# Kernel tuning notes

Measured on AMD Instinct MI355X. Metric: run time of the kernel, lower is better.

Reference implementation:

```python
import jax, jax.numpy as jnp
from jax import lax
import numpy as np

GRID, IMG, BLOCK = 60, 960, 16
BN_EPS = 1e-5


def _conv(x, w, b):
    return lax.conv_general_dilated(x, w, (1, 1), 'SAME', dimension_numbers=('NCHW', 'OIHW', 'NCHW')) + b[None, :, None, None]


def _bn(x, g, b):
    # inference BatchNorm with running_mean=0, running_var=1
    s = g * np.float32(1.0 / np.sqrt(1.0 + BN_EPS))
    return x * s[None, :, None, None] + b[None, :, None, None]


def _mlp(x, w1, b1, w2, b2):
    return jax.nn.relu(x @ w1.T + b1) @ w2.T + b2


def _lstm_layer(x, wih, whh, b):
    # x: [B,T,D]; torch gate order i,f,g,o; zero initial state
    B = x.shape[0]
    H = whh.shape[1]
    pre = jnp.swapaxes(x, 0, 1) @ wih.T + b  # [T,B,4H]

    def step(carry, p):
        h, c = carry
        z = p + h @ whh.T
        i, f, g, o = jnp.split(z, 4, axis=-1)
        c = jax.nn.sigmoid(f) * c + jax.nn.sigmoid(i) * jnp.tanh(g)
        h = jax.nn.sigmoid(o) * jnp.tanh(c)
        return (h, c), h

    z0 = jnp.zeros((B, H), x.dtype)
    (h, c), ys = lax.scan(step, (z0, z0), pre)
    return jnp.swapaxes(ys, 0, 1), h, c


def _forward(motion_vectors, boxes, track_ids, conv1_w, conv1_b, bn1_g, bn1_b, conv2_w, conv2_b, bn2_g, bn2_b, conv3_w, conv3_b, bn3_g, bn3_b, agg_w1, agg_b1, agg_w2, agg_b2, bx_w1, bx_b1, bx_w2, bx_b2, id_table, proj_w, proj_b, empty_slot, l0_wih, l0_whh, l0_b, l1_wih, l1_whh, l1_b, hb_w1, hb_b1, hb_w2, hb_b2, hc_w1, hc_b1, hc_w2, hc_b2, ht_w1, ht_b1, ht_w2, ht_b2):
    B = motion_vectors.shape[0]
    # ---- grid encoder (Conv-BN-ReLU x3) ----
    x = jax.nn.relu(_bn(_conv(motion_vectors, conv1_w, conv1_b), bn1_g, bn1_b))
    x = jax.nn.relu(_bn(_conv(x, conv2_w, conv2_b), bn2_g, bn2_b))
    gf = jax.nn.relu(_bn(_conv(x, conv3_w, conv3_b), bn3_g, bn3_b))  # [B,64,60,60]
    global_feat = gf.mean((-2, -1))  # AdaptiveAvgPool2d(1) -> [B,64]

    # ---- per-box motion statistics (vectorized masked reductions) ----
    bg = jnp.clip(boxes * (IMG / BLOCK), 0.0, GRID - 1e-6)  # grid coords
    ix1 = jnp.floor(bg[..., 0]); iy1 = jnp.floor(bg[..., 1])
    ix2 = jnp.maximum(ix1 + 1.0, jnp.ceil(bg[..., 2]))
    iy2 = jnp.maximum(iy1 + 1.0, jnp.ceil(bg[..., 3]))
    g = jnp.arange(GRID, dtype=bg.dtype)
    mx_ = (g >= ix1[..., None]) & (g < ix2[..., None])  # [B,N,60]
    my_ = (g >= iy1[..., None]) & (g < iy2[..., None])
    mask = my_[..., :, None] & mx_[..., None, :]  # [B,N,60,60]
    m = mask.astype(bg.dtype)
    cnt = m.sum((-2, -1))[..., None]  # [B,N,1], >= 1 by construction
    mv = motion_vectors  # [B,2,60,60]
    s1 = jnp.einsum('bnyx,bcyx->bnc', m, mv)
    s2 = jnp.einsum('bnyx,bcyx->bnc', m, mv * mv)
    mean = s1 / cnt
    var = (s2 - cnt * mean * mean) / jnp.maximum(cnt - 1.0, 1.0)  # unbiased, like torch .std()
    var_safe = jnp.where(cnt > 1.0, jnp.maximum(var, 1e-12), 1.0)
    std = jnp.where(cnt > 1.0, jnp.sqrt(var_safe), 0.0)
    BIG = jnp.asarray(1e9, bg.dtype)
    mn = jnp.min(jnp.where(mask[:, :, None], mv[:, None], BIG), axis=(-2, -1))   # [B,N,2]
    mx = jnp.max(jnp.where(mask[:, :, None], mv[:, None], -BIG), axis=(-2, -1))  # [B,N,2]
    stats = jnp.stack([mean[..., 0], mean[..., 1], std[..., 0], std[..., 1], mn[..., 0], mx[..., 0], mn[..., 1], mx[..., 1]], -1)  # [B,N,8]
    motion_emb = _mlp(stats, agg_w1, agg_b1, agg_w2, agg_b2)  # [B,N,64]

    # ---- slot initialization ----
    box_emb = _mlp(boxes, bx_w1, bx_b1, bx_w2, bx_b2)  # [B,N,64]
    id_emb = id_table[jnp.clip(track_ids, 0, 999)]  # [B,N,32]
    obj = jnp.concatenate([box_emb, id_emb, motion_emb], -1)  # [B,N,160]
    slots = obj @ proj_w.T + proj_b  # [B,300,128]; N == max_slots so no empty slots used

    # ---- 2-layer LSTM over the 300 slots (batch_first, eval -> no dropout) ----
    Ns = slots.shape[1]
    gexp = jnp.broadcast_to(global_feat[:, None, :], (B, Ns, global_feat.shape[-1]))
    lstm_in = jnp.concatenate([slots, gexp], -1)  # [B,300,192]
    y, h0, c0 = _lstm_layer(lstm_in, l0_wih, l0_whh, l0_b)
    y, h1, c1 = _lstm_layer(y, l1_wih, l1_whh, l1_b)  # [B,300,128]

    # ---- RT-DETR style heads ----
    pred_boxes = jax.nn.sigmoid(_mlp(y, hb_w1, hb_b1, hb_w2, hb_b2))  # [B,300,4]
    cls_logits = _mlp(y, hc_w1, hc_b1, hc_w2, hc_b2)  # [B,300,2]
    tid_logits = _mlp(y, ht_w1, ht_b1, ht_w2, ht_b2)  # [B,300,1000]
    h = jnp.stack([h0, h1])
    c = jnp.stack([c0, c1])
    return pred_boxes, cls_logits, tid_logits, h, c


def setup_inputs() -> dict:
    B, N = 32, 300
    key = jax.random.key(0)
    ks = iter(jax.random.split(key, 60))

    def w(*s):
        return jax.random.normal(next(ks), s, jnp.float32) * 0.05

    mv = jax.random.normal(next(ks), (B, 2, GRID, GRID), jnp.float32)
    bb = jax.random.uniform(next(ks), (B, N, 4), jnp.float32)
    boxes = jnp.concatenate([jnp.minimum(bb[..., :2], bb[..., 2:]), jnp.maximum(bb[..., :2], bb[..., 2:])], -1)
    track_ids = jax.random.randint(next(ks), (B, N), 0, 1000)
    return dict(
        motion_vectors=mv, boxes=boxes, track_ids=track_ids,
        conv1_w=w(32, 2, 3, 3), conv1_b=w(32), bn1_g=1.0 + w(32), bn1_b=w(32),
        conv2_w=w(64, 32, 3, 3), conv2_b=w(64), bn2_g=1.0 + w(64), bn2_b=w(64),
        conv3_w=w(64, 64, 3, 3), conv3_b=w(64), bn3_g=1.0 + w(64), bn3_b=w(64),
        agg_w1=w(32, 8), agg_b1=w(32), agg_w2=w(64, 32), agg_b2=w(64),
        bx_w1=w(32, 4), bx_b1=w(32), bx_w2=w(64, 32), bx_b2=w(64),
        id_table=w(1000, 32).at[0].set(0.0),
        proj_w=w(128, 160), proj_b=w(128), empty_slot=w(128),
        l0_wih=w(512, 192), l0_whh=w(512, 128), l0_b=w(512),
        l1_wih=w(512, 128), l1_whh=w(512, 128), l1_b=w(512),
        hb_w1=w(256, 128), hb_b1=w(256), hb_w2=w(4, 256), hb_b2=w(4),
        hc_w1=w(256, 128), hc_b1=w(256), hc_w2=w(2, 256), hc_b2=w(2),
        ht_w1=w(256, 128), ht_b1=w(256), ht_w2=w(1000, 256), ht_b2=w(1000))


def reference(motion_vectors, boxes, track_ids, conv1_w, conv1_b, bn1_g, bn1_b, conv2_w, conv2_b, bn2_g, bn2_b, conv3_w, conv3_b, bn3_g, bn3_b, agg_w1, agg_b1, agg_w2, agg_b2, bx_w1, bx_b1, bx_w2, bx_b2, id_table, proj_w, proj_b, empty_slot, l0_wih, l0_whh, l0_b, l1_wih, l1_whh, l1_b, hb_w1, hb_b1, hb_w2, hb_b2, hc_w1, hc_b1, hc_w2, hc_b2, ht_w1, ht_b1, ht_w2, ht_b2):
    return _forward(motion_vectors, boxes, track_ids, conv1_w, conv1_b, bn1_g, bn1_b, conv2_w, conv2_b, bn2_g, bn2_b, conv3_w, conv3_b, bn3_g, bn3_b, agg_w1, agg_b1, agg_w2, agg_b2, bx_w1, bx_b1, bx_w2, bx_b2, id_table, proj_w, proj_b, empty_slot, l0_wih, l0_whh, l0_b, l1_wih, l1_whh, l1_b, hb_w1, hb_b1, hb_w2, hb_b2, hc_w1, hc_b1, hc_w2, hc_b2, ht_w1, ht_b1, ht_w2, ht_b2)
```

## Files before the change

kernel.cpp:

```cpp
#include <hip/hip_runtime.h>
#include <hip/hip_bf16.h>
#include <math.h>

typedef unsigned short ushort_t;
typedef __attribute__((ext_vector_type(8))) short bf16x8;
typedef __attribute__((ext_vector_type(4))) float f32x4;

__device__ __forceinline__ float sigf(float x) {
  x = fminf(fmaxf(x, -30.f), 30.f);
  return 1.f / (1.f + __expf(-x));
}
__device__ __forceinline__ float sig2(float x) {
  return __builtin_amdgcn_rcpf(1.f + __expf(-x));
}
__device__ __forceinline__ float tanh2(float x) {
  return 1.f - 2.f * __builtin_amdgcn_rcpf(__expf(2.f * x) + 1.f);
}
__device__ __forceinline__ ushort_t f2bf(float x) {
  unsigned int b = __float_as_uint(x);
  unsigned int lsb = (b >> 16) & 1u;
  b += 0x7fffu + lsb;
  return (ushort_t)(b >> 16);
}
__device__ __forceinline__ float bf2f(ushort_t u) {
  return __uint_as_float(((unsigned int)u) << 16);
}

#define NPIX 3600
__device__ __forceinline__ int gperm(int rho) {
  return ((rho & 3) << 7) + (rho >> 2);
}

__global__ __launch_bounds__(256) void wprep_kernel(
    const float* __restrict__ conv2_w, const float* __restrict__ conv3_w,
    const float* __restrict__ wih0,
    const float* __restrict__ projW,
    const float* __restrict__ projb,
    const float* __restrict__ l0_b,
    const float* __restrict__ hbw1, const float* __restrict__ hcw1,
    const float* __restrict__ htw1, const float* __restrict__ htw2,
    const float* __restrict__ hbb1, const float* __restrict__ hcb1,
    const float* __restrict__ htb1, ushort_t* __restrict__ wc2,
    ushort_t* __restrict__ wc3, ushort_t* __restrict__ wAp,
    float* __restrict__ l0bp, ushort_t* __restrict__ whid,
    ushort_t* __restrict__ wt2, float* __restrict__ bhid) {
  int i = blockIdx.x * 256 + threadIdx.x;
  if (i < 18432) {
    int oc = i / 288, r = i % 288, kt = r / 32, ic = r % 32;
    wc2[i] = f2bf(conv2_w[((oc * 32 + ic) * 3 + kt / 3) * 3 + kt % 3]);
    return;
  }
  i -= 18432;
  if (i < 36864) {
    int oc = i / 576, r = i % 576, c = r / 288, r2 = r % 288;
    int kt = r2 / 32, icl = r2 % 32, ic = c * 32 + icl;
    wc3[i] = f2bf(conv3_w[((oc * 64 + ic) * 3 + kt / 3) * 3 + kt % 3]);
    return;
  }
  i -= 36864;
  if (i < 98304) {
    int n = i / 192, k = i % 192;
    int src = gperm(n);
    float a = 0.f;
    if (k < 160) {
      const float* wr = wih0 + src * 192;
      for (int j = 0; j < 128; ++j) a = fmaf(wr[j], projW[j * 160 + k], a);
    }
    wAp[i] = f2bf(a);
    return;
  }
  i -= 98304;
  if (i < 512) {
    int src = gperm(i);
    float a = l0_b[src];
    const float* wr = wih0 + src * 192;
    for (int j = 0; j < 128; ++j) a = fmaf(wr[j], projb[j], a);
    l0bp[i] = a;
    return;
  }
  i -= 512;
  if (i < 98304) {
    int row = i >> 7, c = i & 127;
    float v = (row < 256)   ? hbw1[row * 128 + c]
              : (row < 512) ? hcw1[(row - 256) * 128 + c]
                            : htw1[(row - 512) * 128 + c];
    whid[i] = f2bf(v);
    return;
  }
  i -= 98304;
  if (i < 256000) {
    wt2[i] = f2bf(htw2[i]);
    return;
  }
  i -= 256000;
  if (i < 768)
    bhid[i] = (i < 256) ? hbb1[i] : (i < 512) ? hcb1[i - 256] : htb1[i - 512];
}

__global__ __launch_bounds__(256) void gvec_kernel(
    const float* __restrict__ wih0, const float* __restrict__ gf,
    float* __restrict__ gvec) {
  int i = blockIdx.x * 256 + threadIdx.x;
  int b = i >> 9, n = i & 511;
  const float* wr = wih0 + gperm(n) * 192 + 128;
  const float* g = gf + b * 64;
  float a = 0.f;
#pragma unroll
  for (int k = 0; k < 64; ++k) a = fmaf(wr[k], g[k], a);
  gvec[i] = a * (1.f / 3600.f);
}

__global__ __launch_bounds__(256) void front_kernel(
    const float* __restrict__ mv, const float* __restrict__ c1w,
    const float* __restrict__ c1b, const float* __restrict__ bg1,
    const float* __restrict__ bb1, ushort_t* __restrict__ x1out,
    const float* __restrict__ boxes, const int* __restrict__ ids,
    const float* __restrict__ agg_w1, const float* __restrict__ agg_b1,
    const float* __restrict__ agg_w2, const float* __restrict__ agg_b2,
    const float* __restrict__ bx_w1, const float* __restrict__ bx_b1,
    const float* __restrict__ bx_w2, const float* __restrict__ bx_b2,
    const float* __restrict__ id_table, ushort_t* __restrict__ obj_out) {
  if (blockIdx.x < 14400) {
    int idx = blockIdx.x * 256 + threadIdx.x;
    int x = idx % 60;
    int y = (idx / 60) % 60;
    int oc = (idx / 3600) % 32;
    int b = idx / (3600 * 32);
    float acc = 0.f;
#pragma unroll
    for (int ic = 0; ic < 2; ++ic) {
      const float* src = mv + (b * 2 + ic) * NPIX;
      const float* wp = c1w + (oc * 2 + ic) * 9;
#pragma unroll
      for (int ky = 0; ky < 3; ++ky) {
        int gy = y + ky - 1;
        if (gy < 0 || gy >= 60) continue;
#pragma unroll
        for (int kx = 0; kx < 3; ++kx) {
          int gx = x + kx - 1;
          if (gx < 0 || gx >= 60) continue;
          acc = fmaf(src[gy * 60 + gx], wp[ky * 3 + kx], acc);
        }
      }
    }
    float s = bg1[oc] * rsqrtf(1.f + 1e-5f);
    float v = fmaf(acc, s, fmaf(c1b[oc], s, bb1[oc]));
    x1out[idx] = f2bf(fmaxf(v, 0.f));
    return;
  }
  __shared__ float obj[2][160];
  __shared__ float hm[2][32];
  __shared__ float hbx[2][32];
  __shared__ float stats[2][8];
  __shared__ float boxf[2][4];
  __shared__ float red[2][2][8];
  int h = threadIdx.x >> 7;
  int t = threadIdx.x & 127;
  int blk = (blockIdx.x - 14400) * 2 + h;
  int b = blk / 300;
  float bx0 = boxes[blk * 4 + 0], by0 = boxes[blk * 4 + 1];
  float bx1 = boxes[blk * 4 + 2], by1 = boxes[blk * 4 + 3];
  const float HI = (float)(60.0 - 1e-6);
  float gx1 = fminf(fmaxf(bx0 * 60.f, 0.f), HI);
  float gy1 = fminf(fmaxf(by0 * 60.f, 0.f), HI);
  float gx2 = fminf(fmaxf(bx1 * 60.f, 0.f), HI);
  float gy2 = fminf(fmaxf(by1 * 60.f, 0.f), HI);
  float fx1 = floorf(gx1), fy1 = floorf(gy1);
  float fx2 = fmaxf(fx1 + 1.f, ceilf(gx2));
  float fy2 = fmaxf(fy1 + 1.f, ceilf(gy2));
  int ix1 = (int)fx1, iy1 = (int)fy1, ix2 = (int)fx2, iy2 = (int)fy2;
  int w = ix2 - ix1, hgt = iy2 - iy1;
  int area = w * hgt;
  float s0 = 0.f, s1 = 0.f, q0 = 0.f, q1 = 0.f;
  float mn0 = 1e9f, mn1 = 1e9f, mx0 = -1e9f, mx1 = -1e9f;
  const float* mv0 = mv + b * 2 * NPIX;
  const float* mv1 = mv0 + NPIX;
  for (int i = t; i < area; i += 128) {
    int r = i / w, cc = i - r * w;
    int yy = iy1 + r, xx = ix1 + cc;
    float v0 = mv0[yy * 60 + xx];
    float v1 = mv1[yy * 60 + xx];
    s0 += v0; q0 += v0 * v0; mn0 = fminf(mn0, v0); mx0 = fmaxf(mx0, v0);
    s1 += v1; q1 += v1 * v1; mn1 = fminf(mn1, v1); mx1 = fmaxf(mx1, v1);
  }
#pragma unroll
  for (int off = 32; off; off >>= 1) {
    s0 += __shfl_down(s0, off); s1 += __shfl_down(s1, off);
    q0 += __shfl_down(q0, off); q1 += __shfl_down(q1, off);
    mn0 = fminf(mn0, __shfl_down(mn0, off));
    mn1 = fminf(mn1, __shfl_down(mn1, off));
    mx0 = fmaxf(mx0, __shfl_down(mx0, off));
    mx1 = fmaxf(mx1, __shfl_down(mx1, off));
  }
  if ((t & 63) == 0) {
    int wv = t >> 6;
    red[h][wv][0] = s0; red[h][wv][1] = s1;
    red[h][wv][2] = q0; red[h][wv][3] = q1;
    red[h][wv][4] = mn0; red[h][wv][5] = mn1;
    red[h][wv][6] = mx0; red[h][wv][7] = mx1;
  }
  __syncthreads();
  if (t == 0) {
    float S0 = red[h][0][0] + red[h][1][0], S1 = red[h][0][1] + red[h][1][1];
    float Q0 = red[h][0][2] + red[h][1][2], Q1 = red[h][0][3] + red[h][1][3];
    float MN0 = fminf(red[h][0][4], red[h][1][4]);
    float MN1 = fminf(red[h][0][5], red[h][1][5]);
    float MX0 = fmaxf(red[h][0][6], red[h][1][6]);
    float MX1 = fmaxf(red[h][0][7], red[h][1][7]);
    float cnt = (float)area;
    float mean0 = S0 / cnt, mean1 = S1 / cnt;
    float var0 = (Q0 - cnt * mean0 * mean0) / fmaxf(cnt - 1.f, 1.f);
    float var1 = (Q1 - cnt * mean1 * mean1) / fmaxf(cnt - 1.f, 1.f);
    float sd0 = (cnt > 1.f) ? sqrtf(fmaxf(var0, 1e-12f)) : 0.f;
    float sd1 = (cnt > 1.f) ? sqrtf(fmaxf(var1, 1e-12f)) : 0.f;
    stats[h][0] = mean0; stats[h][1] = mean1; stats[h][2] = sd0;
    stats[h][3] = sd1; stats[h][4] = MN0; stats[h][5] = MX0;
    stats[h][6] = MN1; stats[h][7] = MX1;
    boxf[h][0] = bx0; boxf[h][1] = by0; boxf[h][2] = bx1; boxf[h][3] = by1;
  }
  __syncthreads();
  if (t < 32) {
    float a = agg_b1[t];
#pragma unroll
    for (int k = 0; k < 8; ++k) a = fmaf(stats[h][k], agg_w1[t * 8 + k], a);
    hm[h][t] = fmaxf(a, 0.f);
  } else if (t < 64) {
    int j = t - 32;
    float a = bx_b1[j];
#pragma unroll
    for (int k = 0; k < 4; ++k) a = fmaf(boxf[h][k], bx_w1[j * 4 + k], a);
    hbx[h][j] = fmaxf(a, 0.f);
  }
  __syncthreads();
  if (t < 64) {
    float a = bx_b2[t];
#pragma unroll
    for (int k = 0; k < 32; ++k) a = fmaf(hbx[h][k], bx_w2[t * 32 + k], a);
    obj[h][t] = a;
  } else {
    int j = t - 64;
    float a = agg_b2[j];
#pragma unroll
    for (int k = 0; k < 32; ++k) a = fmaf(hm[h][k], agg_w2[j * 32 + k], a);
    obj[h][96 + j] = a;
  }
  if (t < 32) {
    int id = ids[blk];
    id = min(max(id, 0), 999);
    obj[h][64 + t] = id_table[id * 32 + t];
  }
  __syncthreads();
  obj_out[(size_t)blk * 192 + t] = f2bf(obj[h][t]);
  if (t < 32) {
    obj_out[(size_t)blk * 192 + 128 + t] = f2bf(obj[h][128 + t]);
    obj_out[(size_t)blk * 192 + 160 + t] = 0;
  }
}

template <int CIN, bool POOL>
__global__ __launch_bounds__(256) void conv_mfma_kernel(
    const ushort_t* __restrict__ in, const ushort_t* __restrict__ wc,
    const float* __restrict__ cb, const float* __restrict__ bg,
    const float* __restrict__ bb, ushort_t* __restrict__ out,
    float* __restrict__ gf) {
  constexpr int NCHUNK = CIN / 32;
  __shared__ ushort_t in_lds[18 * 18 * 40];
  int tid = threadIdx.x;
  int wv = tid >> 6, lane = tid & 63;
  int col = lane & 15, kg = lane >> 4;
  int b = blockIdx.y, tile = blockIdx.x;
  int tq = tile >> 2, tr = tile & 3;
  int ty0 = tq * 16 - (tq == 3 ? 4 : 0);
  int tx0 = tr * 16 - (tr == 3 ? 4 : 0);
  int oc = wv * 16 + col;

  bf16x8 bw[NCHUNK * 9];
#pragma unroll
  for (int c = 0; c < NCHUNK; ++c)
#pragma unroll
    for (int kt = 0; kt < 9; ++kt)
      bw[c * 9 + kt] = *(const bf16x8*)(wc + oc * (NCHUNK * 288) + c * 288 +
                                        kt * 32 + kg * 8);

  f32x4 acc[16];
#pragma unroll
  for (int m = 0; m < 16; ++m) acc[m] = (f32x4){0.f, 0.f, 0.f, 0.f};

  for (int c = 0; c < NCHUNK; ++c) {
    if (c) __syncthreads();
    for (int i = tid; i < 18 * 18 * 32; i += 256) {
      int ic = i / 324, rem = i % 324;
      int yy = rem / 18, xx = rem % 18;
      int gy = ty0 + yy - 1, gx = tx0 + xx - 1;
      ushort_t v = 0;
      if (gy >= 0 && gy < 60 && gx >= 0 && gx < 60)
        v = in[((size_t)(b * CIN + c * 32 + ic) * 60 + gy) * 60 + gx];
      in_lds[(yy * 18 + xx) * 40 + ic] = v;
    }
    __syncthreads();
#pragma unroll
    for (int kt = 0; kt < 9; ++kt) {
      int ky = kt / 3, kx = kt % 3;
#pragma unroll
      for (int m = 0; m < 16; ++m) {
        bf16x8 af =
            *(const bf16x8*)(&in_lds[((m + ky) * 18 + col + kx) * 40 + kg * 8]);
        acc[m] = __builtin_amdgcn_mfma_f32_16x16x32_bf16(af, bw[c * 9 + kt],
                                                         acc[m], 0, 0, 0);
      }
    }
  }
  float s = bg[oc] * rsqrtf(1.f + 1e-5f);
  float bias = fmaf(cb[oc], s, bb[oc]);
  float pool = 0.f;
#pragma unroll
  for (int m = 0; m < 16; ++m) {
    float vv[4];
#pragma unroll
    for (int r = 0; r < 4; ++r) vv[r] = fmaxf(fmaf(acc[m][r], s, bias), 0.f);
    if (POOL) {
      bool ymask = (tq != 3) || (m >= 4);
#pragma unroll
      for (int r = 0; r < 4; ++r) {
        int px = kg * 4 + r;
        bool xmask = (tr != 3) || (px >= 4);
        if (ymask && xmask) pool += vv[r];
      }
    } else {
      ushort_t st[4];
#pragma unroll
      for (int r = 0; r < 4; ++r) st[r] = f2bf(vv[r]);
      int yy = ty0 + m, xx = tx0 + kg * 4;
      *(uint2*)(&out[((size_t)(b * 64 + oc) * 60 + yy) * 60 + xx]) =
          *(uint2*)st;
    }
  }
  if (POOL) {
    pool += __shfl_xor(pool, 16);
    pool += __shfl_xor(pool, 32);
    if (lane < 16) atomicAdd(&gf[b * 64 + oc], pool);
  }
}

template <int ACT, bool OBF16, bool GVEC>
__global__ __launch_bounds__(256) void gemm_bf16w_kernel(
    const ushort_t* __restrict__ A, int lda, const ushort_t* __restrict__ W,
    const float* __restrict__ bias, void* __restrict__ C, int ldc, int M,
    int N, int K, const float* __restrict__ gvec) {
  __shared__ ushort_t As[128 * 64];
  __shared__ ushort_t Ws[64 * 64];
  int tid = threadIdx.x;
  int wv = tid >> 6, lane = tid & 63;
  int col = lane & 15, kg = lane >> 4;
  int wm = wv >> 1, wn = wv & 1;
  int m0 = blockIdx.x * 128, n0 = blockIdx.y * 64;
  f32x4 acc[4][2];
#pragma unroll
  for (int i = 0; i < 4; ++i)
#pragma unroll
    for (int j = 0; j < 2; ++j) acc[i][j] = (f32x4){0.f, 0.f, 0.f, 0.f};

  int nk = K >> 6;
  for (int kc = 0; kc < nk; ++kc) {
    if (kc) __syncthreads();
#pragma unroll
    for (int q = 0; q < 4; ++q) {
      int idx = q * 256 + tid;
      int row = idx >> 3, ch = idx & 7;
      uint4 v =
          *(const uint4*)(A + (size_t)(m0 + row) * lda + kc * 64 + ch * 8);
      *(uint4*)(&As[row * 64 + ((ch * 8) ^ ((row & 7) << 3))]) = v;
    }
#pragma unroll
    for (int q = 0; q < 2; ++q) {
      int idx = q * 256 + tid;
      int row = idx >> 3, ch = idx & 7;
      int n = n0 + row;
      uint4 v = make_uint4(0, 0, 0, 0);
      if (n < N) v = *(const uint4*)(W + (size_t)n * K + kc * 64 + ch * 8);
      *(uint4*)(&Ws[row * 64 + ((ch * 8) ^ ((row & 7) << 3))]) = v;
    }
    __syncthreads();
#pragma unroll
    for (int ks = 0; ks < 2; ++ks) {
      bf16x8 bfr[2], afr[4];
#pragma unroll
      for (int ni = 0; ni < 2; ++ni) {
        int row = wn * 32 + ni * 16 + col;
        bfr[ni] = *(const bf16x8*)(
            &Ws[row * 64 + ((ks * 32 + kg * 8) ^ ((row & 7) << 3))]);
      }
#pragma unroll
      for (int mi = 0; mi < 4; ++mi) {
        int row = wm * 64 + mi * 16 + col;
        afr[mi] = *(const bf16x8*)(
            &As[row * 64 + ((ks * 32 + kg * 8) ^ ((row & 7) << 3))]);
      }
#pragma unroll
      for (int mi = 0; mi < 4; ++mi)
#pragma unroll
        for (int ni = 0; ni < 2; ++ni)
          acc[mi][ni] = __builtin_amdgcn_mfma_f32_16x16x32_bf16(
              afr[mi], bfr[ni], acc[mi][ni], 0, 0, 0);
    }
  }
#pragma unroll
  for (int ni = 0; ni < 2; ++ni) {
    int n = n0 + wn * 32 + ni * 16 + col;
    float bn = (n < N) ? bias[n] : 0.f;
#pragma unroll
    for (int mi = 0; mi < 4; ++mi) {
      int mbase = m0 + wm * 64 + mi * 16 + kg * 4;
#pragma unroll
      for (int r = 0; r < 4; ++r) {
        float v = acc[mi][ni][r] + bn;
        if (GVEC) v += gvec[((mbase + r) / 300) * 512 + n];
        if (ACT == 1) v = fmaxf(v, 0.f);
        if (n < N) {
          if (OBF16)
            ((ushort_t*)C)[(size_t)(mbase + r) * ldc + n] = f2bf(v);
          else
            ((float*)C)[(size_t)(mbase + r) * ldc + n] = v;
        }
      }
    }
  }
}

__global__ __launch_bounds__(256) void head_small_kernel(
    const ushort_t* __restrict__ hid, const float* __restrict__ wb2,
    const float* __restrict__ bb2, const float* __restrict__ wc2,
    const float* __restrict__ bc2, float* __restrict__ outB,
    float* __restrict__ outC) {
  int idx = blockIdx.x * 256 + threadIdx.x;
  int row = idx / 6, j = idx % 6;
  const ushort_t* h = hid + (size_t)row * 768 + (j < 4 ? 0 : 256);
  const float* wrow = (j < 4) ? wb2 + j * 256 : wc2 + (j - 4) * 256;
  float acc = (j < 4) ? bb2[j] : bc2[j - 4];
  for (int k = 0; k < 256; k += 8) {
    uint4 hv = *(const uint4*)(h + k);
    unsigned int ww[4] = {hv.x, hv.y, hv.z, hv.w};
#pragma unroll
    for (int q = 0; q < 4; ++q) {
      acc = fmaf(bf2f((ushort_t)(ww[q] & 0xffff)), wrow[k + 2 * q], acc);
      acc = fmaf(bf2f((ushort_t)(ww[q] >> 16)), wrow[k + 2 * q + 1], acc);
    }
  }
  float v = (j < 4) ? sigf(acc) : acc;
  if (j < 4) outB[row * 4 + j] = v;
  else outC[row * 2 + (j - 4)] = v;
}

#define LSTM_BAR() asm volatile("s_waitcnt lgkmcnt(0)\n\ts_barrier" ::: "memory")

__global__ __launch_bounds__(512) void lstm_fused_kernel(
    const float* __restrict__ pre0,
    const float* __restrict__ whh0,
    const float* __restrict__ wih1,
    const float* __restrict__ whh1,
    const float* __restrict__ b1,
    float* __restrict__ pre1,
    ushort_t* __restrict__ y0,
    ushort_t* __restrict__ y1,
    float* __restrict__ outH, float* __restrict__ outC,
    unsigned int* __restrict__ flags)
{
  __shared__ ushort_t h_lds[2][4][160];
  int tid = threadIdx.x;
  int w = tid >> 6, lane = tid & 63;
  int col = lane & 15, kg = lane >> 4;
  int bat = col & 3, q = col >> 2;
  int cell = (4 * w + q) * 4 + kg;

  if (blockIdx.x < 8) {
    int g = blockIdx.x;
    int b0 = g * 4;
    unsigned int* flagp = &flags[g * 32];
    for (int i = tid; i < 2 * 4 * 160; i += 512) ((ushort_t*)h_lds)[i] = 0;
    bf16x8 aW0[4][4];
#pragma unroll
    for (int j = 0; j < 4; ++j) {
      int rho = (4 * w + j) * 16 + col;
      int src = gperm(rho);
#pragma unroll
      for (int kt = 0; kt < 4; ++kt) {
        const float* s1 = whh0 + src * 128 + kt * 32 + kg * 8;
        bf16x8 f1;
#pragma unroll
        for (int qq = 0; qq < 8; ++qq) f1[qq] = (short)f2bf(s1[qq]);
        aW0[j][kt] = f1;
      }
    }
    const float* pg = pre0 + (size_t)(b0 + bat) * 300 * 512 + 4 * cell;
    ushort_t* yg0 = y0 + ((size_t)(b0 + bat) * 300) * 128 + cell;
    float c = 0.f, hout = 0.f;
    f32x4 p0v = *(const f32x4*)(pg);
    f32x4 p1v = *(const f32x4*)(pg + 512);
    __syncthreads();

    for (int s = 0; s < 300; ++s) {
      const ushort_t* hb = h_lds[s & 1][bat];
      bf16x8 bfr[4];
#pragma unroll
      for (int kt = 0; kt < 4; ++kt)
        bfr[kt] = *(const bf16x8*)(hb + kt * 32 + kg * 8);
      f32x4 a0 = {0.f, 0.f, 0.f, 0.f}, a1 = a0, a2 = a0, a3 = a0;
#pragma unroll
      for (int kt = 0; kt < 4; ++kt) {
        a0 = __builtin_amdgcn_mfma_f32_16x16x32_bf16(aW0[0][kt], bfr[kt], a0, 0, 0, 0);
        a1 = __builtin_amdgcn_mfma_f32_16x16x32_bf16(aW0[1][kt], bfr[kt], a1, 0, 0, 0);
        a2 = __builtin_amdgcn_mfma_f32_16x16x32_bf16(aW0[2][kt], bfr[kt], a2, 0, 0, 0);
        a3 = __builtin_amdgcn_mfma_f32_16x16x32_bf16(aW0[3][kt], bfr[kt], a3, 0, 0, 0);
      }
      f32x4 z = a0;
      if (q == 1) z = a1;
      if (q == 2) z = a2;
      if (q == 3) z = a3;
      {
        float zi = z[0] + p0v[0];
        float zf = z[1] + p0v[1];
        float zg = z[2] + p0v[2];
        float zo = z[3] + p0v[3];
        float vi = sig2(zi), vf = sig2(zf), vg = tanh2(zg), vo = sig2(zo);
        c = vf * c + vi * vg;
        hout = vo * tanh2(c);
        ushort_t hv = f2bf(hout);
        h_lds[(s + 1) & 1][bat][cell] = hv;
        __builtin_nontemporal_store(hv, yg0 + (size_t)s * 128);
        p0v = p1v;
        int sn = (s + 2 < 300) ? s + 2 : 299;
        p1v = *(const f32x4*)(pg + (size_t)sn * 512);
      }
      asm volatile("s_waitcnt vmcnt(6)" ::: "memory");
      LSTM_BAR();
      if (tid == 0 && s >= 3)
        __hip_atomic_store(flagp, (unsigned int)(s - 3), __ATOMIC_RELAXED,
                           __HIP_MEMORY_SCOPE_AGENT);
    }
    asm volatile("s_waitcnt vmcnt(0)" ::: "memory");
    __syncthreads();
    if (tid == 0)
      __hip_atomic_store(flagp, 300u, __ATOMIC_RELAXED,
                         __HIP_MEMORY_SCOPE_AGENT);
    outH[(b0 + bat) * 128 + cell] = hout;
    outC[(b0 + bat) * 128 + cell] = c;
  } else if (blockIdx.x < 16) {
    int g = blockIdx.x - 8;
    int b0 = g * 4;
    unsigned int* flagp = &flags[g * 32 + 16];
    for (int i = tid; i < 2 * 4 * 160; i += 512) ((ushort_t*)h_lds)[i] = 0;
    bf16x8 aW[4][4];
#pragma unroll
    for (int j = 0; j < 4; ++j) {
      int rho = (4 * w + j) * 16 + col;
      int src = gperm(rho);
#pragma unroll
      for (int kt = 0; kt < 4; ++kt) {
        const float* s1 = whh1 + src * 128 + kt * 32 + kg * 8;
        bf16x8 f1;
#pragma unroll
        for (int qq = 0; qq < 8; ++qq) f1[qq] = (short)f2bf(s1[qq]);
        aW[j][kt] = f1;
      }
    }
    float bi = b1[cell], bff = b1[128 + cell], bgg = b1[256 + cell],
          boo = b1[384 + cell];
    const float* pg = pre1 + (size_t)(b0 + bat) * 300 * 512 + 4 * cell;
    ushort_t* yg = y1 + (size_t)(b0 + bat) * 300 * 128 + cell;
    float c = 0.f, hout = 0.f;
    unsigned int fc = 0;
    f32x4 p0v, p1v;
    do {
      fc = __hip_atomic_load(flagp, __ATOMIC_RELAXED,
                             __HIP_MEMORY_SCOPE_AGENT);
      if (fc < 1) __builtin_amdgcn_s_sleep(2);
    } while (fc < 1);
    asm volatile("" ::: "memory");
    p0v = __builtin_nontemporal_load((const f32x4*)(pg));
    while (fc < 2) {
      fc = __hip_atomic_load(flagp, __ATOMIC_RELAXED,
                             __HIP_MEMORY_SCOPE_AGENT);
      if (fc < 2) __builtin_amdgcn_s_sleep(2);
    }
    asm volatile("" ::: "memory");
    p1v = __builtin_nontemporal_load((const f32x4*)(pg + 512));
    __syncthreads();

    for (int t = 0; t < 300; ++t) {
      const ushort_t* hb = h_lds[t & 1][bat];
      bf16x8 bfr[4];
#pragma unroll
      for (int kt = 0; kt < 4; ++kt)
        bfr[kt] = *(const bf16x8*)(hb + kt * 32 + kg * 8);
      f32x4 a0 = {0.f, 0.f, 0.f, 0.f}, a1 = a0, a2 = a0, a3 = a0;
#pragma unroll
      for (int kt = 0; kt < 4; ++kt) {
        a0 = __builtin_amdgcn_mfma_f32_16x16x32_bf16(aW[0][kt], bfr[kt], a0, 0, 0, 0);
        a1 = __builtin_amdgcn_mfma_f32_16x16x32_bf16(aW[1][kt], bfr[kt], a1, 0, 0, 0);
        a2 = __builtin_amdgcn_mfma_f32_16x16x32_bf16(aW[2][kt], bfr[kt], a2, 0, 0, 0);
        a3 = __builtin_amdgcn_mfma_f32_16x16x32_bf16(aW[3][kt], bfr[kt], a3, 0, 0, 0);
      }
      f32x4 z = a0;
      if (q == 1) z = a1;
      if (q == 2) z = a2;
      if (q == 3) z = a3;
      {
        float zi = z[0] + p0v[0] + bi;
        float zf = z[1] + p0v[1] + bff;
        float zg = z[2] + p0v[2] + bgg;
        float zo = z[3] + p0v[3] + boo;
        float vi = sig2(zi), vf = sig2(zf), vg = tanh2(zg), vo = sig2(zo);
        c = vf * c + vi * vg;
        hout = vo * tanh2(c);
        ushort_t hv = f2bf(hout);
        h_lds[(t + 1) & 1][bat][cell] = hv;
        yg[(size_t)t * 128] = hv;
        p0v = p1v;
        if (t + 2 < 300) {
          unsigned int need = (unsigned int)(t + 3);
          if (fc < need) {
            do {
              fc = __hip_atomic_load(flagp, __ATOMIC_RELAXED,
                                     __HIP_MEMORY_SCOPE_AGENT);
              if (fc < need) __builtin_amdgcn_s_sleep(2);
            } while (fc < need);
            asm volatile("" ::: "memory");
          }
          p1v = __builtin_nontemporal_load(
              (const f32x4*)(pg + (size_t)(t + 2) * 512));
        }
      }
      LSTM_BAR();
    }
    outH[4096 + (b0 + bat) * 128 + cell] = hout;
    outC[4096 + (b0 + bat) * 128 + cell] = c;
  } else {
    int g = blockIdx.x - 16;
    int b0 = g * 4;
    unsigned int* flag0 = &flags[g * 32];
    unsigned int* flag1 = &flags[g * 32 + 16];
    bf16x8 aU[4][4];
#pragma unroll
    for (int j = 0; j < 4; ++j) {
      int rho = (4 * w + j) * 16 + col;
      int src = gperm(rho);
#pragma unroll
      for (int kt = 0; kt < 4; ++kt) {
        const float* s2 = wih1 + src * 128 + kt * 32 + kg * 8;
        bf16x8 f2;
#pragma unroll
        for (int qq = 0; qq < 8; ++qq) f2[qq] = (short)f2bf(s2[qq]);
        aU[j][kt] = f2;
      }
    }
    int bb = col & 3;
    int ts = col >> 2;
    const ushort_t* yb = y0 + ((size_t)(b0 + bb) * 300) * 128 + kg * 8;
    unsigned int fc = 0;
    for (int t0 = 0; t0 < 300; t0 += 12) {
      unsigned int need = (unsigned int)(t0 + 11);
      while (fc < need) {
        fc = __hip_atomic_load(flag0, __ATOMIC_RELAXED,
                               __HIP_MEMORY_SCOPE_AGENT);
        if (fc < need) __builtin_amdgcn_s_sleep(2);
      }
      asm volatile("" ::: "memory");
      f32x4 acc[4][3];
#pragma unroll
      for (int j = 0; j < 4; ++j)
#pragma unroll
        for (int ct = 0; ct < 3; ++ct) acc[j][ct] = (f32x4){0.f, 0.f, 0.f, 0.f};
#pragma unroll
      for (int ct = 0; ct < 3; ++ct) {
        int t = t0 + ct * 4 + ts;
        bf16x8 bfr[4];
#pragma unroll
        for (int kt = 0; kt < 4; ++kt)
          bfr[kt] = __builtin_nontemporal_load(
              (const bf16x8*)(yb + (size_t)t * 128 + kt * 32));
#pragma unroll
        for (int kt = 0; kt < 4; ++kt) {
          acc[0][ct] = __builtin_amdgcn_mfma_f32_16x16x32_bf16(aU[0][kt], bfr[kt], acc[0][ct], 0, 0, 0);
          acc[1][ct] = __builtin_amdgcn_mfma_f32_16x16x32_bf16(aU[1][kt], bfr[kt], acc[1][ct], 0, 0, 0);
          acc[2][ct] = __builtin_amdgcn_mfma_f32_16x16x32_bf16(aU[2][kt], bfr[kt], acc[2][ct], 0, 0, 0);
          acc[3][ct] = __builtin_amdgcn_mfma_f32_16x16x32_bf16(aU[3][kt], bfr[kt], acc[3][ct], 0, 0, 0);
        }
      }
#pragma unroll
      for (int ct = 0; ct < 3; ++ct) {
        int t = t0 + ct * 4 + ts;
        float* pd = pre1 + ((size_t)(b0 + bb) * 300 + t) * 512 + kg * 4;
#pragma unroll
        for (int j = 0; j < 4; ++j)
          __builtin_nontemporal_store(acc[j][ct],
                                      (f32x4*)(pd + (4 * w + j) * 16));
      }
      asm volatile("s_waitcnt vmcnt(0)" ::: "memory");
      __syncthreads();
      if (tid == 0)
        __hip_atomic_store(flag1, (unsigned int)(t0 + 12), __ATOMIC_RELAXED,
                           __HIP_MEMORY_SCOPE_AGENT);
    }
  }
}

extern "C" void kernel_launch(void* const* d_in, const int* in_sizes, int n_in,
                              void* d_out, int out_size, void* d_ws,
                              size_t ws_size, hipStream_t stream) {
  const float* mv = (const float*)d_in[0];
  const float* boxes = (const float*)d_in[1];
  const int* track_ids = (const int*)d_in[2];
  const float* conv1_w = (const float*)d_in[3];
  const float* conv1_b = (const float*)d_in[4];
  const float* bn1_g = (const float*)d_in[5];
  const float* bn1_b = (const float*)d_in[6];
  const float* conv2_w = (const float*)d_in[7];
  const float* conv2_b = (const float*)d_in[8];
  const float* bn2_g = (const float*)d_in[9];
  const float* bn2_b = (const float*)d_in[10];
  const float* conv3_w = (const float*)d_in[11];
  const float* conv3_b = (const float*)d_in[12];
  const float* bn3_g = (const float*)d_in[13];
  const float* bn3_b = (const float*)d_in[14];
  const float* agg_w1 = (const float*)d_in[15];
  const float* agg_b1 = (const float*)d_in[16];
  const float* agg_w2 = (const float*)d_in[17];
  const float* agg_b2 = (const float*)d_in[18];
  const float* bx_w1 = (const float*)d_in[19];
  const float* bx_b1 = (const float*)d_in[20];
  const float* bx_w2 = (const float*)d_in[21];
  const float* bx_b2 = (const float*)d_in[22];
  const float* id_table = (const float*)d_in[23];
  const float* proj_w = (const float*)d_in[24];
  const float* proj_b = (const float*)d_in[25];
  const float* l0_wih = (const float*)d_in[27];
  const float* l0_whh = (const float*)d_in[28];
  const float* l0_b = (const float*)d_in[29];
  const float* l1_wih = (const float*)d_in[30];
  const float* l1_whh = (const float*)d_in[31];
  const float* l1_b = (const float*)d_in[32];
  const float* hb_w1 = (const float*)d_in[33];
  const float* hb_b1 = (const float*)d_in[34];
  const float* hb_w2 = (const float*)d_in[35];
  const float* hb_b2 = (const float*)d_in[36];
  const float* hc_w1 = (const float*)d_in[37];
  const float* hc_b1 = (const float*)d_in[38];
  const float* hc_w2 = (const float*)d_in[39];
  const float* hc_b2 = (const float*)d_in[40];
  const float* ht_w1 = (const float*)d_in[41];
  const float* ht_b1 = (const float*)d_in[42];
  const float* ht_w2 = (const float*)d_in[43];
  const float* ht_b2 = (const float*)d_in[44];

  char* wsb = (char*)d_ws;
  ushort_t* x1u = (ushort_t*)(wsb + 0);
  ushort_t* x2u = (ushort_t*)(wsb + 7372800);
  float* pre0 = (float*)(wsb + 0);
  ushort_t* hid = (ushort_t*)(wsb + 0);
  ushort_t* y0g = (ushort_t*)(wsb + 19660800);
  float* gf = (float*)(wsb + 22118400);
  ushort_t* obj = (ushort_t*)(wsb + 22126592);
  float* pre1 = (float*)(wsb + 25812992);
  ushort_t* y1b = (ushort_t*)(wsb + 45473792);
  unsigned int* flags = (unsigned int*)(wsb + 47931392);
  ushort_t* wAp = (ushort_t*)(wsb + 47932416);
  ushort_t* whid = (ushort_t*)(wsb + 48129024);
  ushort_t* wt2 = (ushort_t*)(wsb + 48325632);
  float* bhid = (float*)(wsb + 48837632);
  float* l0bp = (float*)(wsb + 48840704);
  float* gvec = (float*)(wsb + 48842752);
  ushort_t* wc2 = (ushort_t*)(wsb + 48908288);
  ushort_t* wc3 = (ushort_t*)(wsb + 48945152);

  float* outB = (float*)d_out;
  float* outC = outB + 38400;
  float* outT = outB + 57600;
  float* outH = outB + 9657600;
  float* outCc = outB + 9665792;

  hipMemsetAsync(gf, 0, 2048 * sizeof(float), stream);
  hipMemsetAsync(flags, 0, 1024, stream);

  wprep_kernel<<<1989, 256, 0, stream>>>(
      conv2_w, conv3_w, l0_wih, proj_w, proj_b, l0_b, hb_w1, hc_w1, ht_w1,
      ht_w2, hb_b1, hc_b1, ht_b1, wc2, wc3, wAp, l0bp, whid, wt2, bhid);
  front_kernel<<<19200, 256, 0, stream>>>(
      mv, conv1_w, conv1_b, bn1_g, bn1_b, x1u, boxes, track_ids, agg_w1,
      agg_b1, agg_w2, agg_b2, bx_w1, bx_b1, bx_w2, bx_b2, id_table, obj);
  conv_mfma_kernel<32, false><<<dim3(16, 32), 256, 0, stream>>>(
      x1u, wc2, conv2_b, bn2_g, bn2_b, x2u, nullptr);
  conv_mfma_kernel<64, true><<<dim3(16, 32), 256, 0, stream>>>(
      x2u, wc3, conv3_b, bn3_g, bn3_b, nullptr, gf);
  gvec_kernel<<<64, 256, 0, stream>>>(l0_wih, gf, gvec);
  gemm_bf16w_kernel<0, false, true><<<dim3(75, 8), 256, 0, stream>>>(
      obj, 192, wAp, l0bp, pre0, 512, 9600, 512, 192, gvec);
  lstm_fused_kernel<<<24, 512, 0, stream>>>(pre0, l0_whh, l1_wih, l1_whh,
                                            l1_b, pre1, y0g, y1b, outH, outCc,
                                            flags);
  gemm_bf16w_kernel<1, true, false><<<dim3(75, 12), 256, 0, stream>>>(
      y1b, 128, whid, bhid, hid, 768, 9600, 768, 128, nullptr);
  head_small_kernel<<<225, 256, 0, stream>>>(hid, hb_w2, hb_b2, hc_w2, hc_b2,
                                             outB, outC);
  gemm_bf16w_kernel<0, false, false><<<dim3(75, 16), 256, 0, stream>>>(
      hid + 512, 768, wt2, ht_b2, outT, 1000, 9600, 1000, 256, nullptr);
}
```

Before: 535.5 us.

## Fold log2e gate scaling into LSTM weights, merge weight prep into front kernel

Pre-scales the layer-0 input projection, bias, global vector and recurrent/input weights of both LSTM layers by log2(e) (2·log2(e) for the g gate), so the gate activations use raw exp2 instead of exp with an implicit multiply on the serial recurrence path. Merges the weight-preparation kernel into the front kernel as extra blocks, removing one launch and letting the two workloads overlap. Layer 1 also issues an early relaxed flag load at the top of each step to hide polling latency. Scaling before bf16 rounding slightly changes numerics.

After: 543.4 us. No clear change (+1.5%).

```diff
diff --git a/kernel.cpp b/kernel.cpp
--- a/kernel.cpp
+++ b/kernel.cpp
@@ -6,15 +6,11 @@
 typedef __attribute__((ext_vector_type(8))) short bf16x8;
 typedef __attribute__((ext_vector_type(4))) float f32x4;
 
+#define LOG2E 1.4426950408889634f
+
 __device__ __forceinline__ float sigf(float x) {
   x = fminf(fmaxf(x, -30.f), 30.f);
   return 1.f / (1.f + __expf(-x));
-}
-__device__ __forceinline__ float sig2(float x) {
-  return __builtin_amdgcn_rcpf(1.f + __expf(-x));
-}
-__device__ __forceinline__ float tanh2(float x) {
-  return 1.f - 2.f * __builtin_amdgcn_rcpf(__expf(2.f * x) + 1.f);
 }
 __device__ __forceinline__ ushort_t f2bf(float x) {
   unsigned int b = __float_as_uint(x);
@@ -25,76 +21,13 @@
 __device__ __forceinline__ float bf2f(ushort_t u) {
   return __uint_as_float(((unsigned int)u) << 16);
 }
+__device__ __forceinline__ float gsc(int g3) {
+  return (g3 == 2) ? (2.f * LOG2E) : LOG2E;
+}
 
 #define NPIX 3600
 __device__ __forceinline__ int gperm(int rho) {
   return ((rho & 3) << 7) + (rho >> 2);
-}
-
-__global__ __launch_bounds__(256) void wprep_kernel(
-    const float* __restrict__ conv2_w, const float* __restrict__ conv3_w,
-    const float* __restrict__ wih0,
-    const float* __restrict__ projW,
-    const float* __restrict__ projb,
-    const float* __restrict__ l0_b,
-    const float* __restrict__ hbw1, const float* __restrict__ hcw1,
-    const float* __restrict__ htw1, const float* __restrict__ htw2,
-    const float* __restrict__ hbb1, const float* __restrict__ hcb1,
-    const float* __restrict__ htb1, ushort_t* __restrict__ wc2,
-    ushort_t* __restrict__ wc3, ushort_t* __restrict__ wAp,
-    float* __restrict__ l0bp, ushort_t* __restrict__ whid,
-    ushort_t* __restrict__ wt2, float* __restrict__ bhid) {
-  int i = blockIdx.x * 256 + threadIdx.x;
-  if (i < 18432) {
-    int oc = i / 288, r = i % 288, kt = r / 32, ic = r % 32;
-    wc2[i] = f2bf(conv2_w[((oc * 32 + ic) * 3 + kt / 3) * 3 + kt % 3]);
-    return;
-  }
-  i -= 18432;
-  if (i < 36864) {
-    int oc = i / 576, r = i % 576, c = r / 288, r2 = r % 288;
-    int kt = r2 / 32, icl = r2 % 32, ic = c * 32 + icl;
-    wc3[i] = f2bf(conv3_w[((oc * 64 + ic) * 3 + kt / 3) * 3 + kt % 3]);
-    return;
-  }
-  i -= 36864;
-  if (i < 98304) {
-    int n = i / 192, k = i % 192;
-    int src = gperm(n);
-    float a = 0.f;
-    if (k < 160) {
-      const float* wr = wih0 + src * 192;
-      for (int j = 0; j < 128; ++j) a = fmaf(wr[j], projW[j * 160 + k], a);
-    }
-    wAp[i] = f2bf(a);
-    return;
-  }
-  i -= 98304;
-  if (i < 512) {
-    int src = gperm(i);
-    float a = l0_b[src];
-    const float* wr = wih0 + src * 192;
-    for (int j = 0; j < 128; ++j) a = fmaf(wr[j], projb[j], a);
-    l0bp[i] = a;
-    return;
-  }
-  i -= 512;
-  if (i < 98304) {
-    int row = i >> 7, c = i & 127;
-    float v = (row < 256)   ? hbw1[row * 128 + c]
-              : (row < 512) ? hcw1[(row - 256) * 128 + c]
-                            : htw1[(row - 512) * 128 + c];
-    whid[i] = f2bf(v);
-    return;
-  }
-  i -= 98304;
-  if (i < 256000) {
-    wt2[i] = f2bf(htw2[i]);
-    return;
-  }
-  i -= 256000;
-  if (i < 768)
-    bhid[i] = (i < 256) ? hbb1[i] : (i < 512) ? hcb1[i - 256] : htb1[i - 512];
 }
 
 __global__ __launch_bounds__(256) void gvec_kernel(
@@ -107,7 +40,7 @@
   float a = 0.f;
 #pragma unroll
   for (int k = 0; k < 64; ++k) a = fmaf(wr[k], g[k], a);
-  gvec[i] = a * (1.f / 3600.f);
+  gvec[i] = a * (1.f / 3600.f) * gsc(n & 3);
 }
 
 __global__ __launch_bounds__(256) void front_kernel(
@@ -119,9 +52,74 @@
     const float* __restrict__ agg_w2, const float* __restrict__ agg_b2,
     const float* __restrict__ bx_w1, const float* __restrict__ bx_b1,
     const float* __restrict__ bx_w2, const float* __restrict__ bx_b2,
-    const float* __restrict__ id_table, ushort_t* __restrict__ obj_out) {
-  if (blockIdx.x < 14400) {
-    int idx = blockIdx.x * 256 + threadIdx.x;
+    const float* __restrict__ id_table, ushort_t* __restrict__ obj_out,
+    const float* __restrict__ conv2_w, const float* __restrict__ conv3_w,
+    const float* __restrict__ wih0, const float* __restrict__ projW,
+    const float* __restrict__ projb, const float* __restrict__ l0_b,
+    const float* __restrict__ hbw1, const float* __restrict__ hcw1,
+    const float* __restrict__ htw1, const float* __restrict__ htw2,
+    const float* __restrict__ hbb1, const float* __restrict__ hcb1,
+    const float* __restrict__ htb1, ushort_t* __restrict__ wc2,
+    ushort_t* __restrict__ wc3, ushort_t* __restrict__ wAp,
+    float* __restrict__ l0bp, ushort_t* __restrict__ whid,
+    ushort_t* __restrict__ wt2, float* __restrict__ bhid) {
+  if (blockIdx.x < 1989) {
+    int i = blockIdx.x * 256 + threadIdx.x;
+    if (i < 18432) {
+      int oc = i / 288, r = i % 288, kt = r / 32, ic = r % 32;
+      wc2[i] = f2bf(conv2_w[((oc * 32 + ic) * 3 + kt / 3) * 3 + kt % 3]);
+      return;
+    }
+    i -= 18432;
+    if (i < 36864) {
+      int oc = i / 576, r = i % 576, c = r / 288, r2 = r % 288;
+      int kt = r2 / 32, icl = r2 % 32, ic = c * 32 + icl;
+      wc3[i] = f2bf(conv3_w[((oc * 64 + ic) * 3 + kt / 3) * 3 + kt % 3]);
+      return;
+    }
+    i -= 36864;
+    if (i < 98304) {
+      int n = i / 192, k = i % 192;
+      int src = gperm(n);
+      float a = 0.f;
+      if (k < 160) {
+        const float* wr = wih0 + src * 192;
+        for (int j = 0; j < 128; ++j) a = fmaf(wr[j], projW[j * 160 + k], a);
+      }
+      wAp[i] = f2bf(a * gsc(n & 3));
+      return;
+    }
+    i -= 98304;
+    if (i < 512) {
+      int src = gperm(i);
+      float a = l0_b[src];
+      const float* wr = wih0 + src * 192;
+      for (int j = 0; j < 128; ++j) a = fmaf(wr[j], projb[j], a);
+      l0bp[i] = a * gsc(i & 3);
+      return;
+    }
+    i -= 512;
+    if (i < 98304) {
+      int row = i >> 7, c = i & 127;
+      float v = (row < 256)   ? hbw1[row * 128 + c]
+                : (row < 512) ? hcw1[(row - 256) * 128 + c]
+                              : htw1[(row - 512) * 128 + c];
+      whid[i] = f2bf(v);
+      return;
+    }
+    i -= 98304;
+    if (i < 256000) {
+      wt2[i] = f2bf(htw2[i]);
+      return;
+    }
+    i -= 256000;
+    if (i < 768)
+      bhid[i] = (i < 256) ? hbb1[i] : (i < 512) ? hcb1[i - 256] : htb1[i - 512];
+    return;
+  }
+  int bx = blockIdx.x - 1989;
+  if (bx < 14400) {
+    int idx = bx * 256 + threadIdx.x;
     int x = idx % 60;
     int y = (idx / 60) % 60;
     int oc = (idx / 3600) % 32;
@@ -156,7 +154,7 @@
   __shared__ float red[2][2][8];
   int h = threadIdx.x >> 7;
   int t = threadIdx.x & 127;
-  int blk = (blockIdx.x - 14400) * 2 + h;
+  int blk = (bx - 14400) * 2 + h;
   int b = blk / 300;
   float bx0 = boxes[blk * 4 + 0], by0 = boxes[blk * 4 + 1];
   float bx1 = boxes[blk * 4 + 2], by1 = boxes[blk * 4 + 3];
@@ -471,6 +469,7 @@
   int col = lane & 15, kg = lane >> 4;
   int bat = col & 3, q = col >> 2;
   int cell = (4 * w + q) * 4 + kg;
+  float wsc = gsc(col & 3);
 
   if (blockIdx.x < 8) {
     int g = blockIdx.x;
@@ -487,7 +486,7 @@
         const float* s1 = whh0 + src * 128 + kt * 32 + kg * 8;
         bf16x8 f1;
 #pragma unroll
-        for (int qq = 0; qq < 8; ++qq) f1[qq] = (short)f2bf(s1[qq]);
+        for (int qq = 0; qq < 8; ++qq) f1[qq] = (short)f2bf(s1[qq] * wsc);
         aW0[j][kt] = f1;
       }
     }
@@ -521,9 +520,14 @@
         float zf = z[1] + p0v[1];
         float zg = z[2] + p0v[2];
         float zo = z[3] + p0v[3];
-        float vi = sig2(zi), vf = sig2(zf), vg = tanh2(zg), vo = sig2(zo);
+        float vi = __builtin_amdgcn_rcpf(1.f + __builtin_amdgcn_exp2f(-zi));
+        float vf = __builtin_amdgcn_rcpf(1.f + __builtin_amdgcn_exp2f(-zf));
+        float vg = 1.f - 2.f * __builtin_amdgcn_rcpf(
+                              __builtin_amdgcn_exp2f(zg) + 1.f);
+        float vo = __builtin_amdgcn_rcpf(1.f + __builtin_amdgcn_exp2f(-zo));
         c = vf * c + vi * vg;
-        hout = vo * tanh2(c);
+        hout = vo * (1.f - 2.f * __builtin_amdgcn_rcpf(
+                             __builtin_amdgcn_exp2f(2.f * LOG2E * c) + 1.f));
         ushort_t hv = f2bf(hout);
         h_lds[(s + 1) & 1][bat][cell] = hv;
         __builtin_nontemporal_store(hv, yg0 + (size_t)s * 128);
@@ -559,12 +563,12 @@
         const float* s1 = whh1 + src * 128 + kt * 32 + kg * 8;
         bf16x8 f1;
 #pragma unroll
-        for (int qq = 0; qq < 8; ++qq) f1[qq] = (short)f2bf(s1[qq]);
+        for (int qq = 0; qq < 8; ++qq) f1[qq] = (short)f2bf(s1[qq] * wsc);
         aW[j][kt] = f1;
       }
     }
-    float bi = b1[cell], bff = b1[128 + cell], bgg = b1[256 + cell],
-          boo = b1[384 + cell];
+    float bi = b1[cell] * LOG2E, bff = b1[128 + cell] * LOG2E;
+    float bgg = b1[256 + cell] * (2.f * LOG2E), boo = b1[384 + cell] * LOG2E;
     const float* pg = pre1 + (size_t)(b0 + bat) * 300 * 512 + 4 * cell;
     ushort_t* yg = y1 + (size_t)(b0 + bat) * 300 * 128 + cell;
     float c = 0.f, hout = 0.f;
@@ -587,6 +591,8 @@
     __syncthreads();
 
     for (int t = 0; t < 300; ++t) {
+      unsigned int fcn = __hip_atomic_load(flagp, __ATOMIC_RELAXED,
+                                           __HIP_MEMORY_SCOPE_AGENT);
       const ushort_t* hb = h_lds[t & 1][bat];
       bf16x8 bfr[4];
 #pragma unroll
@@ -609,15 +615,21 @@
         float zf = z[1] + p0v[1] + bff;
         float zg = z[2] + p0v[2] + bgg;
         float zo = z[3] + p0v[3] + boo;
-        float vi = sig2(zi), vf = sig2(zf), vg = tanh2(zg), vo = sig2(zo);
+        float vi = __builtin_amdgcn_rcpf(1.f + __builtin_amdgcn_exp2f(-zi));
+        float vf = __builtin_amdgcn_rcpf(1.f + __builtin_amdgcn_exp2f(-zf));
+        float vg = 1.f - 2.f * __builtin_amdgcn_rcpf(
+                              __builtin_amdgcn_exp2f(zg) + 1.f);
+        float vo = __builtin_amdgcn_rcpf(1.f + __builtin_amdgcn_exp2f(-zo));
         c = vf * c + vi * vg;
-        hout = vo * tanh2(c);
+        hout = vo * (1.f - 2.f * __builtin_amdgcn_rcpf(
+                             __builtin_amdgcn_exp2f(2.f * LOG2E * c) + 1.f));
         ushort_t hv = f2bf(hout);
         h_lds[(t + 1) & 1][bat][cell] = hv;
         yg[(size_t)t * 128] = hv;
         p0v = p1v;
         if (t + 2 < 300) {
           unsigned int need = (unsigned int)(t + 3);
+          if (fcn > fc) fc = fcn;
           if (fc < need) {
             do {
               fc = __hip_atomic_load(flagp, __ATOMIC_RELAXED,
@@ -649,7 +661,7 @@
         const float* s2 = wih1 + src * 128 + kt * 32 + kg * 8;
         bf16x8 f2;
 #pragma unroll
-        for (int qq = 0; qq < 8; ++qq) f2[qq] = (short)f2bf(s2[qq]);
+        for (int qq = 0; qq < 8; ++qq) f2[qq] = (short)f2bf(s2[qq] * wsc);
         aU[j][kt] = f2;
       }
     }
@@ -781,12 +793,11 @@
   hipMemsetAsync(gf, 0, 2048 * sizeof(float), stream);
   hipMemsetAsync(flags, 0, 1024, stream);
 
-  wprep_kernel<<<1989, 256, 0, stream>>>(
+  front_kernel<<<21189, 256, 0, stream>>>(
+      mv, conv1_w, conv1_b, bn1_g, bn1_b, x1u, boxes, track_ids, agg_w1,
+      agg_b1, agg_w2, agg_b2, bx_w1, bx_b1, bx_w2, bx_b2, id_table, obj,
       conv2_w, conv3_w, l0_wih, proj_w, proj_b, l0_b, hb_w1, hc_w1, ht_w1,
       ht_w2, hb_b1, hc_b1, ht_b1, wc2, wc3, wAp, l0bp, whid, wt2, bhid);
-  front_kernel<<<19200, 256, 0, stream>>>(
-      mv, conv1_w, conv1_b, bn1_g, bn1_b, x1u, boxes, track_ids, agg_w1,
-      agg_b1, agg_w2, agg_b2, bx_w1, bx_b1, bx_w2, bx_b2, id_table, obj);
   conv_mfma_kernel<32, false><<<dim3(16, 32), 256, 0, stream>>>(
       x1u, wc2, conv2_b, bn2_g, bn2_b, x2u, nullptr);
   conv_mfma_kernel<64, true><<<dim3(16, 32), 256, 0, stream>>>(
```
